# Optimization experiments

Hardware: AMD Instinct MI355X
Metric: run time of the kernel (lower is better)

Reference implementation:

```python
import jax, jax.numpy as jnp
import numpy as np

N_BEST = 50          # hypotheses per utterance segment
NUM_SEG = 1_000_000  # number of utterance segments
TOTAL = N_BEST * NUM_SEG


def setup_inputs() -> dict:
    key = jax.random.key(0)
    scores = jax.random.normal(key, (TOTAL,), dtype=jnp.float32)
    # per-segment n-best counts; sum(nBestIndex) == len(scores)
    nBestIndex = jnp.full((NUM_SEG,), N_BEST, dtype=jnp.int32)
    return {"scores": scores, "nBestIndex": nBestIndex}


def reference(scores, nBestIndex):
    # Segmented (ragged) softmax: softmax within each contiguous n-best group.
    # Equivalent to the torch loop with log_score=False, fused into one pass.
    num_seg = nBestIndex.shape[0]
    total = scores.shape[0]
    # segment id for each score element
    seg = jnp.repeat(jnp.arange(num_seg, dtype=jnp.int32), nBestIndex,
                     total_repeat_length=total)
    # numerically stable segmented softmax
    seg_max = jax.ops.segment_max(scores, seg, num_segments=num_seg)
    exps = jnp.exp(scores - seg_max[seg])
    seg_sum = jax.ops.segment_sum(exps, seg, num_segments=num_seg)
    return exps / seg_sum[seg]
```

## Files before the change

kernel.cpp:

```cpp
#include <hip/hip_runtime.h>
#include <math.h>


#define SEGS 256
#define BLOCK 512
#define LDS_FLOATS 12928

__global__ __launch_bounds__(256) void scan_local_kernel(
    const int* __restrict__ counts, int n_seg,
    int* __restrict__ local_scan, int* __restrict__ block_sums) {
    __shared__ int sm[256];
    const int t = threadIdx.x;
    const int g = blockIdx.x * 256 + t;
    const int v = (g < n_seg) ? counts[g] : 0;
    sm[t] = v;
    __syncthreads();
    for (int off = 1; off < 256; off <<= 1) {
        int y = (t >= off) ? sm[t - off] : 0;
        __syncthreads();
        sm[t] += y;
        __syncthreads();
    }
    if (g < n_seg) local_scan[g] = sm[t] - v;
    if (t == 255) block_sums[blockIdx.x] = sm[255];
}

__global__ __launch_bounds__(256) void scan_bsums_kernel(
    int* __restrict__ bsum, int nb) {
    __shared__ int sm[256];
    const int t = threadIdx.x;
    const int per = (nb + 255) >> 8;
    const int beg = t * per;
    const int end = (beg + per < nb) ? beg + per : nb;
    int tot = 0;
    for (int j = beg; j < end; ++j) tot += bsum[j];
    sm[t] = tot;
    __syncthreads();
    for (int off = 1; off < 256; off <<= 1) {
        int y = (t >= off) ? sm[t - off] : 0;
        __syncthreads();
        sm[t] += y;
        __syncthreads();
    }
    int run = sm[t] - tot;
    for (int j = beg; j < end; ++j) {
        int v = bsum[j];
        bsum[j] = run;
        run += v;
    }
}

__global__ __launch_bounds__(BLOCK) void seg_softmax_kernel(
    const float* __restrict__ scores,
    const int* __restrict__ local_scan, const int* __restrict__ bsum,
    float* __restrict__ out, int n_seg, int total) {
    __shared__ float sm[LDS_FLOATS];
    __shared__ int starts[SEGS + 1];

    const int tid  = threadIdx.x;
    const int seg0 = blockIdx.x * SEGS;

    if (tid <= SEGS) {
        const int seg = seg0 + tid;
        starts[tid] = (seg < n_seg) ? (local_scan[seg] + bsum[seg >> 8]) : total;
    }
    __syncthreads();

    const int base = starts[0];
    const int span = starts[SEGS] - base;

    if (span <= LDS_FLOATS && (base & 3) == 0) {
        const float4* __restrict__ src = (const float4*)(scores + base);
        const int nvec = span >> 2;
        for (int i = tid; i < nvec; i += BLOCK)
            ((float4*)sm)[i] = src[i];
        for (int i = (nvec << 2) + tid; i < span; i += BLOCK)
            sm[i] = scores[base + i];
        __syncthreads();

        if (tid < SEGS) {
            const int s0 = starts[tid] - base;
            const int c  = starts[tid + 1] - starts[tid];
            if (c > 0) {
                float m = -INFINITY;
                for (int j = 0; j < c; ++j)
                    m = fmaxf(m, sm[s0 + j]);
                float s = 0.0f;
                for (int j = 0; j < c; ++j) {
                    const float e = __expf(sm[s0 + j] - m);
                    sm[s0 + j] = e;
                    s += e;
                }
                const float inv = 1.0f / s;
                for (int j = 0; j < c; ++j)
                    sm[s0 + j] *= inv;
            }
        }
        __syncthreads();

        float4* __restrict__ dst = (float4*)(out + base);
        for (int i = tid; i < nvec; i += BLOCK)
            dst[i] = ((const float4*)sm)[i];
        for (int i = (nvec << 2) + tid; i < span; i += BLOCK)
            out[base + i] = sm[i];
    } else {
        if (tid < SEGS) {
            const int seg = seg0 + tid;
            if (seg < n_seg) {
                const int st = starts[tid];
                const int c  = starts[tid + 1] - st;
                if (c > 0) {
                    float m = -INFINITY;
                    for (int j = 0; j < c; ++j)
                        m = fmaxf(m, scores[st + j]);
                    float s = 0.0f;
                    for (int j = 0; j < c; ++j)
                        s += __expf(scores[st + j] - m);
                    const float inv = 1.0f / s;
                    for (int j = 0; j < c; ++j)
                        out[st + j] = __expf(scores[st + j] - m) * inv;
                }
            }
        }
    }
}

extern "C" void kernel_launch(void* const* d_in, const int* in_sizes, int n_in,
                              void* d_out, int out_size, void* d_ws, size_t ws_size,
                              hipStream_t stream) {
    const float* scores = (const float*)d_in[0];
    const int*   counts = (const int*)d_in[1];
    float* out = (float*)d_out;
    const int n_seg = in_sizes[1];
    const int total = in_sizes[0];

    int* local_scan = (int*)d_ws;
    const int nblocksA = (n_seg + 255) / 256;
    int* block_sums = local_scan + n_seg;

    scan_local_kernel<<<nblocksA, 256, 0, stream>>>(counts, n_seg, local_scan, block_sums);
    scan_bsums_kernel<<<1, 256, 0, stream>>>(block_sums, nblocksA);

    const int nblocksC = (n_seg + SEGS - 1) / SEGS;
    seg_softmax_kernel<<<nblocksC, BLOCK, 0, stream>>>(
        scores, local_scan, block_sums, out, n_seg, total);
}
```

Baseline: 358.2 us.

## Assign 16-lane groups per segment with shuffle reductions instead of LDS staging

Replaces the thread-per-segment softmax, which staged a 256-segment span in LDS, with a scheme where 16 lanes cooperate on each segment. Values are held in registers (up to 64 per segment) and max and sum are reduced with xor shuffles. This removes the LDS footprint that limited occupancy and the serial per-thread loops over 50 elements. Global loads are scalar and strided by lane rather than float4, so coalescing relies on neighbouring groups covering adjacent addresses.

```diff
diff --git a/kernel.cpp b/kernel.cpp
--- a/kernel.cpp
+++ b/kernel.cpp
@@ -2,9 +2,9 @@
 #include <math.h>
 
 
-#define SEGS 256
-#define BLOCK 512
-#define LDS_FLOATS 12928
+#define GSEG 16
+#define SBLOCK 256
+#define SEG_PER_BLOCK (SBLOCK / GSEG)
 
 __global__ __launch_bounds__(256) void scan_local_kernel(
     const int* __restrict__ counts, int n_seg,
@@ -50,78 +50,67 @@
     }
 }
 
-__global__ __launch_bounds__(BLOCK) void seg_softmax_kernel(
+__global__ __launch_bounds__(SBLOCK) void seg_softmax_kernel(
     const float* __restrict__ scores,
     const int* __restrict__ local_scan, const int* __restrict__ bsum,
     float* __restrict__ out, int n_seg, int total) {
-    __shared__ float sm[LDS_FLOATS];
-    __shared__ int starts[SEGS + 1];
+    const int tid = threadIdx.x;
+    const int p   = tid & (GSEG - 1);
+    const int seg = blockIdx.x * SEG_PER_BLOCK + (tid >> 4);
+    if (seg >= n_seg) return;
 
-    const int tid  = threadIdx.x;
-    const int seg0 = blockIdx.x * SEGS;
+    const int st = local_scan[seg] + bsum[seg >> 8];
+    int en;
+    if (seg + 1 < n_seg) en = local_scan[seg + 1] + bsum[(seg + 1) >> 8];
+    else                 en = total;
+    const int c = en - st;
+    if (c <= 0) return;
 
-    if (tid <= SEGS) {
-        const int seg = seg0 + tid;
-        starts[tid] = (seg < n_seg) ? (local_scan[seg] + bsum[seg >> 8]) : total;
-    }
-    __syncthreads();
+    if (c <= 4 * GSEG) {
+        const int i0 = p, i1 = p + GSEG, i2 = p + 2 * GSEG, i3 = p + 3 * GSEG;
+        float v0 = -INFINITY, v1 = -INFINITY, v2 = -INFINITY, v3 = -INFINITY;
+        if (i0 < c) v0 = scores[st + i0];
+        if (i1 < c) v1 = scores[st + i1];
+        if (i2 < c) v2 = scores[st + i2];
+        if (i3 < c) v3 = scores[st + i3];
 
-    const int base = starts[0];
-    const int span = starts[SEGS] - base;
+        float m = fmaxf(fmaxf(v0, v1), fmaxf(v2, v3));
+        #pragma unroll
+        for (int off = 1; off < GSEG; off <<= 1)
+            m = fmaxf(m, __shfl_xor(m, off, GSEG));
 
-    if (span <= LDS_FLOATS && (base & 3) == 0) {
-        const float4* __restrict__ src = (const float4*)(scores + base);
-        const int nvec = span >> 2;
-        for (int i = tid; i < nvec; i += BLOCK)
-            ((float4*)sm)[i] = src[i];
-        for (int i = (nvec << 2) + tid; i < span; i += BLOCK)
-            sm[i] = scores[base + i];
-        __syncthreads();
+        v0 = __expf(v0 - m);
+        v1 = __expf(v1 - m);
+        v2 = __expf(v2 - m);
+        v3 = __expf(v3 - m);
+        float s = (v0 + v1) + (v2 + v3);
+        #pragma unroll
+        for (int off = 1; off < GSEG; off <<= 1)
+            s += __shfl_xor(s, off, GSEG);
 
-        if (tid < SEGS) {
-            const int s0 = starts[tid] - base;
-            const int c  = starts[tid + 1] - starts[tid];
-            if (c > 0) {
-                float m = -INFINITY;
-                for (int j = 0; j < c; ++j)
-                    m = fmaxf(m, sm[s0 + j]);
-                float s = 0.0f;
-                for (int j = 0; j < c; ++j) {
-                    const float e = __expf(sm[s0 + j] - m);
-                    sm[s0 + j] = e;
-                    s += e;
-                }
-                const float inv = 1.0f / s;
-                for (int j = 0; j < c; ++j)
-                    sm[s0 + j] *= inv;
-            }
-        }
-        __syncthreads();
+        const float inv = 1.0f / s;
+        if (i0 < c) out[st + i0] = v0 * inv;
+        if (i1 < c) out[st + i1] = v1 * inv;
+        if (i2 < c) out[st + i2] = v2 * inv;
+        if (i3 < c) out[st + i3] = v3 * inv;
+    } else {
+        float m = -INFINITY;
+        for (int j = p; j < c; j += GSEG)
+            m = fmaxf(m, scores[st + j]);
+        #pragma unroll
+        for (int off = 1; off < GSEG; off <<= 1)
+            m = fmaxf(m, __shfl_xor(m, off, GSEG));
 
-        float4* __restrict__ dst = (float4*)(out + base);
-        for (int i = tid; i < nvec; i += BLOCK)
-            dst[i] = ((const float4*)sm)[i];
-        for (int i = (nvec << 2) + tid; i < span; i += BLOCK)
-            out[base + i] = sm[i];
-    } else {
-        if (tid < SEGS) {
-            const int seg = seg0 + tid;
-            if (seg < n_seg) {
-                const int st = starts[tid];
-                const int c  = starts[tid + 1] - st;
-                if (c > 0) {
-                    float m = -INFINITY;
-                    for (int j = 0; j < c; ++j)
-                        m = fmaxf(m, scores[st + j]);
-                    float s = 0.0f;
-                    for (int j = 0; j < c; ++j)
-                        s += __expf(scores[st + j] - m);
-                    const float inv = 1.0f / s;
-                    for (int j = 0; j < c; ++j)
-                        out[st + j] = __expf(scores[st + j] - m) * inv;
-                }
-            }
-        }
+        float s = 0.0f;
+        for (int j = p; j < c; j += GSEG)
+            s += __expf(scores[st + j] - m);
+        #pragma unroll
+        for (int off = 1; off < GSEG; off <<= 1)
+            s += __shfl_xor(s, off, GSEG);
+
+        const float inv = 1.0f / s;
+        for (int j = p; j < c; j += GSEG)
+            out[st + j] = __expf(scores[st + j] - m) * inv;
     }
 }
 
@@ -141,7 +130,7 @@
     scan_local_kernel<<<nblocksA, 256, 0, stream>>>(counts, n_seg, local_scan, block_sums);
     scan_bsums_kernel<<<1, 256, 0, stream>>>(block_sums, nblocksA);
 
-    const int nblocksC = (n_seg + SEGS - 1) / SEGS;
-    seg_softmax_kernel<<<nblocksC, BLOCK, 0, stream>>>(
+    const int nblocksC = (n_seg + SEG_PER_BLOCK - 1) / SEG_PER_BLOCK;
+    seg_softmax_kernel<<<nblocksC, SBLOCK, 0, stream>>>(
         scores, local_scan, block_sums, out, n_seg, total);
 }
```

After: 352.9 us. Within noise of the previous version (-1.5%).
